# Kernel tuning notes

Hardware: AMD Instinct MI355X
Metric: run time of the kernel (lower is better)

## Reference

```python
import jax, jax.numpy as jnp
import numpy as np

B, S, D, DOUT = 16, 1024, 768, 256
TEMP = D ** 0.5


def setup_inputs() -> dict:
    key = jax.random.key(0)
    ks = jax.random.split(key, 16)
    emb = jax.random.normal(ks[0], (B, S, D), dtype=jnp.float32)
    mask = jax.random.randint(ks[1], (B, S), 0, 2, dtype=jnp.int32)
    scale = 0.02
    def lin(kw, kb, din, dout):
        return (jax.random.normal(kw, (din, dout), dtype=jnp.float32) * scale,
                jax.random.normal(kb, (dout,), dtype=jnp.float32) * scale)
    q_Wq, q_bq = lin(ks[2], ks[3], D, D)
    q_Wk, q_bk = lin(ks[4], ks[5], D, D)
    q_Wv, q_bv = lin(ks[6], ks[7], D, DOUT)
    d_Wq, d_bq = lin(ks[8], ks[9], D, D)
    d_Wk, d_bk = lin(ks[10], ks[11], D, D)
    d_Wv, d_bv = lin(ks[12], ks[13], D, DOUT)
    return {
        'emb': emb, 'mask': mask, 'is_query': 1,
        'query_Wq': q_Wq, 'query_bq': q_bq,
        'query_Wk': q_Wk, 'query_bk': q_bk,
        'query_Wv': q_Wv, 'query_bv': q_bv,
        'doc_Wq': d_Wq, 'doc_bq': d_bq,
        'doc_Wk': d_Wk, 'doc_bk': d_bk,
        'doc_Wv': d_Wv, 'doc_bv': d_bv,
    }


def reference(emb, mask, is_query,
              query_Wq, query_bq, query_Wk, query_bk, query_Wv, query_bv,
              doc_Wq, doc_bq, doc_Wk, doc_bk, doc_Wv, doc_bv):
    # is_query is a static Python int/bool selecting the projection set
    if is_query:
        Wq, bq, Wk, bk, Wv, bv = query_Wq, query_bq, query_Wk, query_bk, query_Wv, query_bv
    else:
        Wq, bq, Wk, bk, Wv, bv = doc_Wq, doc_bq, doc_Wk, doc_bk, doc_Wv, doc_bv
    q = jnp.einsum('bsd,de->bse', emb, Wq) + bq  # [B,S,D]
    k = jnp.einsum('bsd,de->bse', emb, Wk) + bk  # [B,S,D]
    v = jnp.einsum('bsd,de->bse', emb, Wv) + bv  # [B,S,DOUT]
    attn = jnp.einsum('bqd,bkd->bqk', q / TEMP, k)  # [B,S,S]
    attn = jnp.where(mask[:, None, :] == 0, jnp.float32(-1e9), attn)
    attn = jax.nn.softmax(attn, axis=-1)
    out = jnp.einsum('bqk,bkd->bqd', attn, v)  # [B,S,DOUT]
    return out, attn
```

## Files before the change

kernel.cpp:

```cpp
#include <hip/hip_runtime.h>
#include <hip/hip_bf16.h>

static constexpr float INV_TEMP = 0.03608439182435161f;

typedef __attribute__((ext_vector_type(8))) short bf16x8;
typedef __attribute__((ext_vector_type(4))) float f32x4;
typedef __attribute__((ext_vector_type(8))) unsigned short u16x8;
typedef __attribute__((ext_vector_type(4))) unsigned short u16x4;

__device__ __forceinline__ unsigned short f2bf(float f) {
  unsigned u = __float_as_uint(f);
  u += 0x7fffu + ((u >> 16) & 1u);
  return (unsigned short)(u >> 16);
}
__device__ __forceinline__ float bf2f(unsigned short h) {
  return __uint_as_float((unsigned)h << 16);
}

__device__ __forceinline__ void async_copy16(const void* g, void* lds) {
  __builtin_amdgcn_global_load_lds(
      (const __attribute__((address_space(1))) unsigned int*)g,
      (__attribute__((address_space(3))) unsigned int*)lds, 16, 0, 0);
}

__global__ __launch_bounds__(256) void pack_emb(const float* __restrict__ src,
                                                unsigned short* __restrict__ QKE) {
  long i = ((long)blockIdx.x * 256 + threadIdx.x) * 8;
  const long row = i / 768, col = i % 768;
  float4 a = *(const float4*)(src + i);
  float4 b = *(const float4*)(src + i + 4);
  u16x8 v;
  v[0] = f2bf(a.x); v[1] = f2bf(a.y); v[2] = f2bf(a.z); v[3] = f2bf(a.w);
  v[4] = f2bf(b.x); v[5] = f2bf(b.y); v[6] = f2bf(b.z); v[7] = f2bf(b.w);
  *(u16x8*)(QKE + row * 1536 + 768 + col) = v;
}

__global__ __launch_bounds__(256) void pack_sel(
    const int* __restrict__ isq_p,
    const float* qWq, const float* qWk, const float* qWv, const float* qbv,
    const float* dWq, const float* dWk, const float* dWv, const float* dbv,
    unsigned short* __restrict__ Wq_bf,
    unsigned short* __restrict__ Wk_bf,
    unsigned short* __restrict__ WvTe,
    float* __restrict__ bias_v) {
  const int b = blockIdx.x, t = threadIdx.x;
  const int isq = *isq_p;
  if (b < 1152) {
    const int which = b >= 576;
    const float* W = which ? (isq ? qWk : dWk) : (isq ? qWq : dWq);
    unsigned short* o = which ? Wk_bf : Wq_bf;
    const long i = ((long)(which ? b - 576 : b) * 256 + t) * 4;
    float4 x = *(const float4*)(W + i);
    u16x4 y; y[0] = f2bf(x.x); y[1] = f2bf(x.y); y[2] = f2bf(x.z); y[3] = f2bf(x.w);
    *(u16x4*)(o + i) = y;
  } else if (b < 1344) {
    const float* Wv = isq ? qWv : dWv;
    const long base = ((long)(b - 1152) * 256 + t) * 4;
#pragma unroll
    for (int j = 0; j < 4; ++j) {
      long o = base + j;
      int n = (int)(o / 768), d = (int)(o % 768);
      WvTe[o] = f2bf(Wv[(long)d * 256 + n]);
    }
  } else {
    const float* bv = isq ? qbv : dbv;
    if (t < 256) bias_v[t] = bv[t];
  }
}

__global__ __launch_bounds__(256) void gemm_g(
    const unsigned short* __restrict__ Wk_bf,
    const unsigned short* __restrict__ Wq_bf,
    unsigned short* __restrict__ Gt) {
  __shared__ unsigned short Ab[2][64 * 32];
  __shared__ unsigned short Bb[2][64 * 32];
  const int tid = threadIdx.x, wid = tid >> 6, lane = tid & 63;
  const unsigned short* A = Wk_bf + (long)blockIdx.x * 64 * 768;
  const unsigned short* BT = Wq_bf + (long)blockIdx.y * 64 * 768;

  auto stage = [&](int buf, int kt) {
    const int e = tid * 8, row = e >> 5, col = e & 31;
    async_copy16(A + (long)row * 768 + kt * 32 + col, &Ab[buf][e]);
    async_copy16(BT + (long)row * 768 + kt * 32 + col, &Bb[buf][e]);
  };

  f32x4 acc[2][2] = {};
  stage(0, 0);
  __syncthreads();
  int buf = 0;
  const int wr = wid >> 1, wc = wid & 1;
  const int fr = lane & 15, fq = lane >> 4;
  for (int kt = 0; kt < 24; ++kt) {
    if (kt + 1 < 24) stage(buf ^ 1, kt + 1);
    const unsigned short* Ap = &Ab[buf][(wr * 32 + fr) * 32 + fq * 8];
    const unsigned short* Bp = &Bb[buf][(wc * 32 + fr) * 32 + fq * 8];
    bf16x8 a[2], b[2];
#pragma unroll
    for (int mi = 0; mi < 2; ++mi) a[mi] = *(const bf16x8*)(Ap + mi * 16 * 32);
#pragma unroll
    for (int ni = 0; ni < 2; ++ni) b[ni] = *(const bf16x8*)(Bp + ni * 16 * 32);
#pragma unroll
    for (int mi = 0; mi < 2; ++mi)
#pragma unroll
      for (int ni = 0; ni < 2; ++ni)
        acc[mi][ni] = __builtin_amdgcn_mfma_f32_16x16x32_bf16(a[mi], b[ni], acc[mi][ni], 0, 0, 0);
    __syncthreads();
    buf ^= 1;
  }
#pragma unroll
  for (int mi = 0; mi < 2; ++mi)
#pragma unroll
    for (int ni = 0; ni < 2; ++ni) {
      const long m = (long)blockIdx.x * 64 + wr * 32 + mi * 16 + fq * 4;
      const long n = (long)blockIdx.y * 64 + wc * 32 + ni * 16 + fr;
      f32x4 v = acc[mi][ni];
#pragma unroll
      for (int r = 0; r < 4; ++r) Gt[(m + r) * 768 + n] = f2bf(v[r]);
    }
}

__global__ __launch_bounds__(256) void uvc_fast(
    const int* __restrict__ isq_p,
    const float* qWq, const float* qbq, const float* qWk, const float* qbk,
    const float* dWq, const float* dbq, const float* dWk, const float* dbk,
    unsigned short* __restrict__ WvTe, float* __restrict__ bias_v) {
  const int b = blockIdx.x, t = threadIdx.x;
  const int isq = *isq_p;
  const float* Wq = isq ? qWq : dWq;  const float* bq = isq ? qbq : dbq;
  const float* Wk = isq ? qWk : dWk;  const float* bk = isq ? qbk : dbk;
  __shared__ float red[256];
  if (b < 1536) {
    const int lo = (b < 768);
    const int d = lo ? b : b - 768;
    const float* W = lo ? Wq : Wk;
    const float* bvec = lo ? bk : bq;
    float s = 0.f;
#pragma unroll
    for (int i = 0; i < 3; ++i) {
      const int a = t + i * 256;
      s += W[(long)d * 768 + a] * bvec[a];
    }
    red[t] = s;
    __syncthreads();
    for (int off = 128; off; off >>= 1) {
      if (t < off) red[t] += red[t + off];
      __syncthreads();
    }
    if (t == 0) WvTe[(long)(lo ? 256 : 257) * 768 + d] = f2bf(red[0]);
  } else {
    if (t < 128) bias_v[256 + t] = 0.f;
    float p = 0.f;
    for (int a = t; a < 768; a += 256) p += bq[a] * bk[a];
    red[t] = p;
    __syncthreads();
    for (int off = 128; off; off >>= 1) {
      if (t < off) red[t] += red[t + off];
      __syncthreads();
    }
    if (t == 0) bias_v[256] = red[0];
  }
}

__device__ __forceinline__ void k_loop_256(
    const unsigned short* __restrict__ Apan, long lda,
    const unsigned short* __restrict__ Bpan, long ldb,
    int nk, unsigned short* smem, f32x4 (&acc)[8][4]) {
  const int tid = threadIdx.x;
  const int wid = tid >> 6, lane = tid & 63;
  const int wr = wid >> 2, wc = wid & 3;
  const int fr = lane & 15, fq = lane >> 4;

  auto stage = [&](int tile, int mat, int ks, int buf) {
    const unsigned short* g = (mat ? Bpan : Apan) + (long)tile * 64 + ks * 32;
    const long ld = mat ? ldb : lda;
    unsigned short* d = smem + (((buf << 2) | (mat << 1) | ks) << 13);
#pragma unroll
    for (int i = 0; i < 2; ++i) {
      const int e = (tid + i * 512) * 8;
      const int row = e >> 5;
      const int sl = (e >> 3) & 3;
      const int ss = sl ^ ((row >> 1) & 3);
      async_copy16(g + (long)row * ld + ss * 8, d + e);
    }
  };

  const int fro = fr * 32 + ((fq ^ ((fr >> 1) & 3)) << 3);
  const int awo = fro + (wr * 128) * 32;
  const int bwo = fro + (wc * 64) * 32;

  stage(0, 0, 0, 0); stage(0, 1, 0, 0); stage(0, 0, 1, 0); stage(0, 1, 1, 0);
  if (nk > 1) {
    stage(1, 0, 0, 1); stage(1, 1, 1, 1);
    asm volatile("s_waitcnt vmcnt(4)" ::: "memory");
  } else {
    asm volatile("s_waitcnt vmcnt(0)" ::: "memory");
  }
  __builtin_amdgcn_sched_barrier(0);
  __builtin_amdgcn_s_barrier();

  for (int t = 0; t < nk; ++t) {
    const int p = t & 1;
    const unsigned short* A0 = smem + (((p << 2) | 0) << 13);
    const unsigned short* A1 = smem + (((p << 2) | 1) << 13);
    const unsigned short* B0 = smem + (((p << 2) | 2) << 13);
    const unsigned short* B1 = smem + (((p << 2) | 3) << 13);
    bf16x8 a[4], b[4];

#pragma unroll
    for (int m = 0; m < 4; ++m) a[m] = *(const bf16x8*)(A0 + awo + m * 512);
#pragma unroll
    for (int n = 0; n < 4; ++n) b[n] = *(const bf16x8*)(B0 + bwo + n * 512);
    if (t + 1 < nk) stage(t + 1, 0, 1, (t + 1) & 1);
    __builtin_amdgcn_s_barrier();
    asm volatile("s_waitcnt lgkmcnt(0)");
    __builtin_amdgcn_sched_barrier(0);
    __builtin_amdgcn_s_setprio(1);
#pragma unroll
    for (int m = 0; m < 4; ++m)
#pragma unroll
      for (int n = 0; n < 4; ++n)
        acc[m][n] = __builtin_amdgcn_mfma_f32_16x16x32_bf16(a[m], b[n], acc[m][n], 0, 0, 0);
    __builtin_amdgcn_s_setprio(0);
    __builtin_amdgcn_sched_barrier(0);
    __builtin_amdgcn_s_barrier();

#pragma unroll
    for (int m = 0; m < 4; ++m) a[m] = *(const bf16x8*)(A0 + awo + (4 + m) * 512);
    if (t + 1 < nk) stage(t + 1, 1, 0, (t + 1) & 1);
    __builtin_amdgcn_s_barrier();
    asm volatile("s_waitcnt lgkmcnt(0)");
    __builtin_amdgcn_sched_barrier(0);
    __builtin_amdgcn_s_setprio(1);
#pragma unroll
    for (int m = 0; m < 4; ++m)
#pragma unroll
      for (int n = 0; n < 4; ++n)
        acc[4 + m][n] = __builtin_amdgcn_mfma_f32_16x16x32_bf16(a[m], b[n], acc[4 + m][n], 0, 0, 0);
    __builtin_amdgcn_s_setprio(0);
    __builtin_amdgcn_sched_barrier(0);
    __builtin_amdgcn_s_barrier();

#pragma unroll
    for (int m = 0; m < 4; ++m) a[m] = *(const bf16x8*)(A1 + awo + m * 512);
#pragma unroll
    for (int n = 0; n < 4; ++n) b[n] = *(const bf16x8*)(B1 + bwo + n * 512);
    if (t + 2 < nk) stage(t + 2, 0, 0, p);
    __builtin_amdgcn_s_barrier();
    asm volatile("s_waitcnt lgkmcnt(0)");
    __builtin_amdgcn_sched_barrier(0);
    __builtin_amdgcn_s_setprio(1);
#pragma unroll
    for (int m = 0; m < 4; ++m)
#pragma unroll
      for (int n = 0; n < 4; ++n)
        acc[m][n] = __builtin_amdgcn_mfma_f32_16x16x32_bf16(a[m], b[n], acc[m][n], 0, 0, 0);
    __builtin_amdgcn_s_setprio(0);
    __builtin_amdgcn_sched_barrier(0);
    __builtin_amdgcn_s_barrier();

#pragma unroll
    for (int m = 0; m < 4; ++m) a[m] = *(const bf16x8*)(A1 + awo + (4 + m) * 512);
    if (t + 2 < nk) stage(t + 2, 1, 1, p);
    __builtin_amdgcn_s_barrier();
    asm volatile("s_waitcnt lgkmcnt(0)");
    __builtin_amdgcn_sched_barrier(0);
    __builtin_amdgcn_s_setprio(1);
#pragma unroll
    for (int m = 0; m < 4; ++m)
#pragma unroll
      for (int n = 0; n < 4; ++n)
        acc[4 + m][n] = __builtin_amdgcn_mfma_f32_16x16x32_bf16(a[m], b[n], acc[4 + m][n], 0, 0, 0);
    __builtin_amdgcn_s_setprio(0);
    if (t < nk - 2) {
      asm volatile("s_waitcnt vmcnt(4)" ::: "memory");
    } else if (t == nk - 2) {
      asm volatile("s_waitcnt vmcnt(0)" ::: "memory");
    }
    __builtin_amdgcn_sched_barrier(0);
    __builtin_amdgcn_s_barrier();
  }
}

__global__ __launch_bounds__(512, 2) void tproj256(
    unsigned short* __restrict__ QKE,
    const unsigned short* __restrict__ Gt) {
  extern __shared__ unsigned short smem[];
  const int f = blockIdx.x;
  const int kx = f & 7, c = f >> 3;
  const long bx = 8 * kx + (c & 7);
  const long yb = c >> 3;
  const unsigned short* Apan = QKE + 768 + bx * 256 * 1536;
  const unsigned short* Bpan = Gt + yb * 256 * 768;
  f32x4 acc[8][4];
#pragma unroll
  for (int m = 0; m < 8; ++m)
#pragma unroll
    for (int n = 0; n < 4; ++n) acc[m][n] = f32x4{0.f, 0.f, 0.f, 0.f};

  k_loop_256(Apan, 1536, Bpan, 768, 12, smem, acc);

  const int wid = threadIdx.x >> 6, lane = threadIdx.x & 63;
  const int wr = wid >> 2, wc = wid & 3;
  const int fr = lane & 15, fq = lane >> 4;
#pragma unroll
  for (int m = 0; m < 8; ++m)
#pragma unroll
    for (int n = 0; n < 4; ++n) {
      const long mm = bx * 256 + wr * 128 + m * 16 + fq * 4;
      const long nn = yb * 256 + wc * 64 + n * 16 + fr;
      f32x4 v = acc[m][n];
#pragma unroll
      for (int r = 0; r < 4; ++r) QKE[(mm + r) * 1536 + nn] = f2bf(v[r]);
    }
}

__global__ __launch_bounds__(512, 2) void logits256(
    const unsigned short* __restrict__ QKE,
    const unsigned short* __restrict__ VTe,
    float* __restrict__ attn) {
  extern __shared__ unsigned short smem[];
  const int f = blockIdx.x;
  const int kx = f & 7, c = f >> 3;
  const int bz = 2 * kx + (c >> 4);
  const int inner = c & 15, bx = inner & 3, by = inner >> 2;
  const unsigned short* Apan = QKE + (long)bz * 1024 * 1536 + (long)bx * 256 * 1536;
  const unsigned short* Bpan = QKE + 768 + (long)bz * 1024 * 1536 + (long)by * 256 * 1536;
  f32x4 acc[8][4];
#pragma unroll
  for (int m = 0; m < 8; ++m)
#pragma unroll
    for (int n = 0; n < 4; ++n) acc[m][n] = f32x4{0.f, 0.f, 0.f, 0.f};

  k_loop_256(Apan, 1536, Bpan, 1536, 12, smem, acc);

  const int wid = threadIdx.x >> 6, lane = threadIdx.x & 63;
  const int wr = wid >> 2, wc = wid & 3;
  const int fr = lane & 15, fq = lane >> 4;
  float* C = attn + (long)bz * 1024 * 1024;
  const unsigned short* rvec = VTe + (long)256 * 16384 + (long)bz * 1024;
  const unsigned short* cvec = VTe + (long)257 * 16384 + (long)bz * 1024;
#pragma unroll
  for (int m = 0; m < 8; ++m)
#pragma unroll
    for (int n = 0; n < 4; ++n) {
      const long mm = (long)bx * 256 + wr * 128 + m * 16 + fq * 4;
      const long nn = (long)by * 256 + wc * 64 + n * 16 + fr;
      const float cB = bf2f(cvec[nn]);
      f32x4 v = acc[m][n];
#pragma unroll
      for (int r = 0; r < 4; ++r) {
        const float rA = bf2f(rvec[mm + r]);
        C[(mm + r) * 1024 + nn] = (v[r] + rA + cB) * INV_TEMP;
      }
    }
}

__global__ __launch_bounds__(256) void gemm_vt(
    const unsigned short* __restrict__ WvTe,
    const unsigned short* __restrict__ QKE,
    const float* __restrict__ bias_v,
    unsigned short* __restrict__ VTe) {
  __shared__ unsigned short Ab[2][128 * 32];
  __shared__ unsigned short Bb[2][128 * 32];
  const int tid = threadIdx.x, wid = tid >> 6, lane = tid & 63;
  const unsigned short* A = WvTe + (long)blockIdx.x * 128 * 768;
  const unsigned short* BT = QKE + 768 + (long)blockIdx.y * 128 * 1536;
  const int srow = lane >> 2;
  const int skk = (lane & 3) * 8;

  auto stage = [&](int buf, int kt) {
    const unsigned short* As = A + (long)kt * 32;
    const unsigned short* Bs = BT + (long)kt * 32;
#pragma unroll
    for (int i = 0; i < 2; ++i) {
      int c = wid * 2 + i;
      async_copy16(As + (long)(c * 16 + srow) * 768 + skk, &Ab[buf][c * 512]);
      async_copy16(Bs + (long)(c * 16 + srow) * 1536 + skk, &Bb[buf][c * 512]);
    }
  };

  f32x4 acc[4][4] = {};
  stage(0, 0);
  __syncthreads();
  int buf = 0;
  const int wr = wid >> 1, wc = wid & 1;
  const int fr = lane & 15, fq = lane >> 4;
  for (int kt = 0; kt < 24; ++kt) {
    if (kt + 1 < 24) stage(buf ^ 1, kt + 1);
    const unsigned short* Ap = &Ab[buf][(wr * 64 + fr) * 32 + fq * 8];
    const unsigned short* Bp = &Bb[buf][(wc * 64 + fr) * 32 + fq * 8];
    bf16x8 af[4], bfv[4];
#pragma unroll
    for (int mi = 0; mi < 4; ++mi) af[mi] = *(const bf16x8*)(Ap + mi * 16 * 32);
#pragma unroll
    for (int ni = 0; ni < 4; ++ni) bfv[ni] = *(const bf16x8*)(Bp + ni * 16 * 32);
#pragma unroll
    for (int mi = 0; mi < 4; ++mi)
#pragma unroll
      for (int ni = 0; ni < 4; ++ni)
        acc[mi][ni] = __builtin_amdgcn_mfma_f32_16x16x32_bf16(af[mi], bfv[ni], acc[mi][ni], 0, 0, 0);
    __syncthreads();
    buf ^= 1;
  }
#pragma unroll
  for (int mi = 0; mi < 4; ++mi)
#pragma unroll
    for (int ni = 0; ni < 4; ++ni) {
      const long m = (long)blockIdx.x * 128 + wr * 64 + mi * 16 + fq * 4;
      const long n = (long)blockIdx.y * 128 + wc * 64 + ni * 16 + fr;
      f32x4 v = acc[mi][ni];
#pragma unroll
      for (int r = 0; r < 4; ++r)
        VTe[(m + r) * 16384 + n] = f2bf(v[r] + bias_v[m + r]);
    }
}

__global__ __launch_bounds__(256) void softmax_rows(float* __restrict__ attn,
                                                    const int* __restrict__ mask,
                                                    unsigned short* __restrict__ attn_bf) {
  const int row = blockIdx.x;
  const int b = row >> 10;
  float* p = attn + (long)row * 1024;
  const int tid = threadIdx.x, lane = tid & 63, wid = tid >> 6;
  float4 v = ((const float4*)p)[tid];
  int4 mk = ((const int4*)(mask + b * 1024))[tid];
  v.x = mk.x ? v.x : -1e9f;
  v.y = mk.y ? v.y : -1e9f;
  v.z = mk.z ? v.z : -1e9f;
  v.w = mk.w ? v.w : -1e9f;
  float mx = fmaxf(fmaxf(v.x, v.y), fmaxf(v.z, v.w));
#pragma unroll
  for (int off = 32; off; off >>= 1) mx = fmaxf(mx, __shfl_xor(mx, off));
  __shared__ float red[4];
  if (lane == 0) red[wid] = mx;
  __syncthreads();
  mx = fmaxf(fmaxf(red[0], red[1]), fmaxf(red[2], red[3]));
  float e0 = __expf(v.x - mx), e1 = __expf(v.y - mx);
  float e2 = __expf(v.z - mx), e3 = __expf(v.w - mx);
  float s = e0 + e1 + e2 + e3;
#pragma unroll
  for (int off = 32; off; off >>= 1) s += __shfl_xor(s, off);
  __shared__ float red2[4];
  if (lane == 0) red2[wid] = s;
  __syncthreads();
  s = red2[0] + red2[1] + red2[2] + red2[3];
  const float inv = 1.0f / s;
  float4 o;
  o.x = e0 * inv; o.y = e1 * inv; o.z = e2 * inv; o.w = e3 * inv;
  ((float4*)p)[tid] = o;
  u16x4 ob;
  ob[0] = f2bf(o.x); ob[1] = f2bf(o.y); ob[2] = f2bf(o.z); ob[3] = f2bf(o.w);
  *(u16x4*)(attn_bf + (long)row * 1024 + tid * 4) = ob;
}

__global__ __launch_bounds__(256) void gemm_pv(
    const unsigned short* __restrict__ attnbf,
    const unsigned short* __restrict__ VTe,
    float* __restrict__ out) {
  __shared__ unsigned short Ab[2][128 * 32];
  __shared__ unsigned short Bb[2][64 * 32];
  const int tid = threadIdx.x, wid = tid >> 6, lane = tid & 63;
  const int bz = blockIdx.z;
  const unsigned short* A = attnbf + (long)bz * 1024 * 1024 + (long)blockIdx.x * 128 * 1024;
  const unsigned short* BT = VTe + (long)bz * 1024 + (long)blockIdx.y * 64 * 16384;
  const int srow = lane >> 2;
  const int skk = (lane & 3) * 8;

  auto stage = [&](int buf, int kt) {
    const unsigned short* As = A + (long)kt * 32;
    const unsigned short* Bs = BT + (long)kt * 32;
#pragma unroll
    for (int i = 0; i < 2; ++i) {
      int c = wid * 2 + i;
      async_copy16(As + (long)(c * 16 + srow) * 1024 + skk, &Ab[buf][c * 512]);
    }
    async_copy16(Bs + (long)(wid * 16 + srow) * 16384 + skk, &Bb[buf][wid * 512]);
  };

  f32x4 acc[4][2] = {};
  stage(0, 0);
  __syncthreads();
  int buf = 0;
  const int wr = wid >> 1, wc = wid & 1;
  const int fr = lane & 15, fq = lane >> 4;
  for (int kt = 0; kt < 32; ++kt) {
    if (kt + 1 < 32) stage(buf ^ 1, kt + 1);
    const unsigned short* Ap = &Ab[buf][(wr * 64 + fr) * 32 + fq * 8];
    const unsigned short* Bp = &Bb[buf][(wc * 32 + fr) * 32 + fq * 8];
    bf16x8 af[4], bfv[2];
#pragma unroll
    for (int mi = 0; mi < 4; ++mi) af[mi] = *(const bf16x8*)(Ap + mi * 16 * 32);
#pragma unroll
    for (int ni = 0; ni < 2; ++ni) bfv[ni] = *(const bf16x8*)(Bp + ni * 16 * 32);
#pragma unroll
    for (int mi = 0; mi < 4; ++mi)
#pragma unroll
      for (int ni = 0; ni < 2; ++ni)
        acc[mi][ni] = __builtin_amdgcn_mfma_f32_16x16x32_bf16(af[mi], bfv[ni], acc[mi][ni], 0, 0, 0);
    __syncthreads();
    buf ^= 1;
  }

  float* C = out + (long)bz * 1024 * 256;
  const long m0 = (long)blockIdx.x * 128 + wr * 64;
  const long n0 = (long)blockIdx.y * 64 + wc * 32;
#pragma unroll
  for (int mi = 0; mi < 4; ++mi)
#pragma unroll
    for (int ni = 0; ni < 2; ++ni) {
      const long m = m0 + mi * 16 + fq * 4;
      const long n = n0 + ni * 16 + fr;
      f32x4 v = acc[mi][ni];
#pragma unroll
      for (int r = 0; r < 4; ++r) C[(m + r) * 256 + n] = v[r];
    }
}

extern "C" void kernel_launch(void* const* d_in, const int* in_sizes, int n_in,
                              void* d_out, int out_size, void* d_ws, size_t ws_size,
                              hipStream_t stream) {
  const float* emb = (const float*)d_in[0];
  const int* mask = (const int*)d_in[1];
  const int* isq = (const int*)d_in[2];
  const float* qWq = (const float*)d_in[3];  const float* qbq = (const float*)d_in[4];
  const float* qWk = (const float*)d_in[5];  const float* qbk = (const float*)d_in[6];
  const float* qWv = (const float*)d_in[7];  const float* qbv = (const float*)d_in[8];
  const float* dWq = (const float*)d_in[9];  const float* dbq = (const float*)d_in[10];
  const float* dWk = (const float*)d_in[11]; const float* dbk = (const float*)d_in[12];
  const float* dWv = (const float*)d_in[13]; const float* dbv = (const float*)d_in[14];

  char* ws = (char*)d_ws;
  unsigned short* QKE    = (unsigned short*)ws;  ws += (size_t)16384 * 1536 * 2;
  unsigned short* Wq_bf  = (unsigned short*)ws;  ws += (size_t)768 * 768 * 2;
  unsigned short* Wk_bf  = (unsigned short*)ws;  ws += (size_t)768 * 768 * 2;
  unsigned short* WvTe   = (unsigned short*)ws;  ws += (size_t)384 * 768 * 2;
  unsigned short* Gt     = (unsigned short*)ws;  ws += (size_t)768 * 768 * 2;
  float*          bias_v = (float*)ws;           ws += (size_t)384 * 4;
  unsigned short* VTe    = (unsigned short*)ws;  ws += (size_t)384 * 16384 * 2;
  unsigned short* attnbf = (unsigned short*)ws;  ws += (size_t)16 * 1024 * 1024 * 2;

  float* out = (float*)d_out;
  float* attn = out + (size_t)16 * 1024 * 256;

  (void)hipFuncSetAttribute((const void*)&tproj256,
                            hipFuncAttributeMaxDynamicSharedMemorySize, 131072);
  (void)hipFuncSetAttribute((const void*)&logits256,
                            hipFuncAttributeMaxDynamicSharedMemorySize, 131072);

  hipLaunchKernelGGL(pack_emb, dim3(6144), dim3(256), 0, stream, emb, QKE);
  hipLaunchKernelGGL(pack_sel, dim3(1345), dim3(256), 0, stream, isq,
                     qWq, qWk, qWv, qbv, dWq, dWk, dWv, dbv, Wq_bf, Wk_bf, WvTe, bias_v);
  hipLaunchKernelGGL(gemm_g, dim3(12, 12), dim3(256), 0, stream, Wk_bf, Wq_bf, Gt);
  hipLaunchKernelGGL(uvc_fast, dim3(1537), dim3(256), 0, stream, isq,
                     qWq, qbq, qWk, qbk, dWq, dbq, dWk, dbk, WvTe, bias_v);
  hipLaunchKernelGGL(tproj256, dim3(192), dim3(512), 131072, stream, QKE, Gt);
  hipLaunchKernelGGL(gemm_vt, dim3(3, 128), dim3(256), 0, stream,
                     WvTe, QKE, bias_v, VTe);
  hipLaunchKernelGGL(logits256, dim3(256), dim3(512), 131072, stream, QKE, VTe, attn);
  hipLaunchKernelGGL(softmax_rows, dim3(16384), dim3(256), 0, stream, attn, mask, attnbf);
  hipLaunchKernelGGL(gemm_pv, dim3(8, 4, 16), dim3(256), 0, stream, attnbf, VTe, out);
}
```

Baseline: 167.7 us.

## Replace 256x256 hand-pipelined GEMMs with simpler 128x128 double-buffered kernels

Swaps the tproj and logits kernels, previously 512-thread 256x256-tile kernels with a hand-scheduled pipeline and 128KB of dynamic LDS, for 256-thread 128x128-tile kernels using static 32KB double-buffered LDS and a plain sync-per-k-step loop. The grids grow from 192/256 blocks to 768/1024, which gives better CU coverage and occupancy on a 256-CU part. In exchange each tile has less reuse, and the loop drops the fine-grained barrier, priority and waitcnt interleaving, so it may hide global-load latency less well.

```diff
diff --git a/kernel.cpp b/kernel.cpp
--- a/kernel.cpp
+++ b/kernel.cpp
@@ -161,196 +161,133 @@
   }
 }
 
-__device__ __forceinline__ void k_loop_256(
-    const unsigned short* __restrict__ Apan, long lda,
-    const unsigned short* __restrict__ Bpan, long ldb,
-    int nk, unsigned short* smem, f32x4 (&acc)[8][4]) {
-  const int tid = threadIdx.x;
-  const int wid = tid >> 6, lane = tid & 63;
-  const int wr = wid >> 2, wc = wid & 3;
-  const int fr = lane & 15, fq = lane >> 4;
-
-  auto stage = [&](int tile, int mat, int ks, int buf) {
-    const unsigned short* g = (mat ? Bpan : Apan) + (long)tile * 64 + ks * 32;
-    const long ld = mat ? ldb : lda;
-    unsigned short* d = smem + (((buf << 2) | (mat << 1) | ks) << 13);
-#pragma unroll
-    for (int i = 0; i < 2; ++i) {
-      const int e = (tid + i * 512) * 8;
-      const int row = e >> 5;
-      const int sl = (e >> 3) & 3;
-      const int ss = sl ^ ((row >> 1) & 3);
-      async_copy16(g + (long)row * ld + ss * 8, d + e);
-    }
-  };
-
-  const int fro = fr * 32 + ((fq ^ ((fr >> 1) & 3)) << 3);
-  const int awo = fro + (wr * 128) * 32;
-  const int bwo = fro + (wc * 64) * 32;
-
-  stage(0, 0, 0, 0); stage(0, 1, 0, 0); stage(0, 0, 1, 0); stage(0, 1, 1, 0);
-  if (nk > 1) {
-    stage(1, 0, 0, 1); stage(1, 1, 1, 1);
-    asm volatile("s_waitcnt vmcnt(4)" ::: "memory");
-  } else {
-    asm volatile("s_waitcnt vmcnt(0)" ::: "memory");
-  }
-  __builtin_amdgcn_sched_barrier(0);
-  __builtin_amdgcn_s_barrier();
-
-  for (int t = 0; t < nk; ++t) {
-    const int p = t & 1;
-    const unsigned short* A0 = smem + (((p << 2) | 0) << 13);
-    const unsigned short* A1 = smem + (((p << 2) | 1) << 13);
-    const unsigned short* B0 = smem + (((p << 2) | 2) << 13);
-    const unsigned short* B1 = smem + (((p << 2) | 3) << 13);
-    bf16x8 a[4], b[4];
-
-#pragma unroll
-    for (int m = 0; m < 4; ++m) a[m] = *(const bf16x8*)(A0 + awo + m * 512);
-#pragma unroll
-    for (int n = 0; n < 4; ++n) b[n] = *(const bf16x8*)(B0 + bwo + n * 512);
-    if (t + 1 < nk) stage(t + 1, 0, 1, (t + 1) & 1);
-    __builtin_amdgcn_s_barrier();
-    asm volatile("s_waitcnt lgkmcnt(0)");
-    __builtin_amdgcn_sched_barrier(0);
-    __builtin_amdgcn_s_setprio(1);
-#pragma unroll
-    for (int m = 0; m < 4; ++m)
-#pragma unroll
-      for (int n = 0; n < 4; ++n)
-        acc[m][n] = __builtin_amdgcn_mfma_f32_16x16x32_bf16(a[m], b[n], acc[m][n], 0, 0, 0);
-    __builtin_amdgcn_s_setprio(0);
-    __builtin_amdgcn_sched_barrier(0);
-    __builtin_amdgcn_s_barrier();
-
-#pragma unroll
-    for (int m = 0; m < 4; ++m) a[m] = *(const bf16x8*)(A0 + awo + (4 + m) * 512);
-    if (t + 1 < nk) stage(t + 1, 1, 0, (t + 1) & 1);
-    __builtin_amdgcn_s_barrier();
-    asm volatile("s_waitcnt lgkmcnt(0)");
-    __builtin_amdgcn_sched_barrier(0);
-    __builtin_amdgcn_s_setprio(1);
-#pragma unroll
-    for (int m = 0; m < 4; ++m)
-#pragma unroll
-      for (int n = 0; n < 4; ++n)
-        acc[4 + m][n] = __builtin_amdgcn_mfma_f32_16x16x32_bf16(a[m], b[n], acc[4 + m][n], 0, 0, 0);
-    __builtin_amdgcn_s_setprio(0);
-    __builtin_amdgcn_sched_barrier(0);
-    __builtin_amdgcn_s_barrier();
-
-#pragma unroll
-    for (int m = 0; m < 4; ++m) a[m] = *(const bf16x8*)(A1 + awo + m * 512);
-#pragma unroll
-    for (int n = 0; n < 4; ++n) b[n] = *(const bf16x8*)(B1 + bwo + n * 512);
-    if (t + 2 < nk) stage(t + 2, 0, 0, p);
-    __builtin_amdgcn_s_barrier();
-    asm volatile("s_waitcnt lgkmcnt(0)");
-    __builtin_amdgcn_sched_barrier(0);
-    __builtin_amdgcn_s_setprio(1);
-#pragma unroll
-    for (int m = 0; m < 4; ++m)
-#pragma unroll
-      for (int n = 0; n < 4; ++n)
-        acc[m][n] = __builtin_amdgcn_mfma_f32_16x16x32_bf16(a[m], b[n], acc[m][n], 0, 0, 0);
-    __builtin_amdgcn_s_setprio(0);
-    __builtin_amdgcn_sched_barrier(0);
-    __builtin_amdgcn_s_barrier();
-
-#pragma unroll
-    for (int m = 0; m < 4; ++m) a[m] = *(const bf16x8*)(A1 + awo + (4 + m) * 512);
-    if (t + 2 < nk) stage(t + 2, 1, 1, p);
-    __builtin_amdgcn_s_barrier();
-    asm volatile("s_waitcnt lgkmcnt(0)");
-    __builtin_amdgcn_sched_barrier(0);
-    __builtin_amdgcn_s_setprio(1);
-#pragma unroll
-    for (int m = 0; m < 4; ++m)
-#pragma unroll
-      for (int n = 0; n < 4; ++n)
-        acc[4 + m][n] = __builtin_amdgcn_mfma_f32_16x16x32_bf16(a[m], b[n], acc[4 + m][n], 0, 0, 0);
-    __builtin_amdgcn_s_setprio(0);
-    if (t < nk - 2) {
-      asm volatile("s_waitcnt vmcnt(4)" ::: "memory");
-    } else if (t == nk - 2) {
-      asm volatile("s_waitcnt vmcnt(0)" ::: "memory");
-    }
-    __builtin_amdgcn_sched_barrier(0);
-    __builtin_amdgcn_s_barrier();
-  }
-}
-
-__global__ __launch_bounds__(512, 2) void tproj256(
+__global__ __launch_bounds__(256) void tproj2(
     unsigned short* __restrict__ QKE,
     const unsigned short* __restrict__ Gt) {
-  extern __shared__ unsigned short smem[];
+  __shared__ unsigned short Ab[2][128 * 32];
+  __shared__ unsigned short Bb[2][128 * 32];
+  const int tid = threadIdx.x, wid = tid >> 6, lane = tid & 63;
   const int f = blockIdx.x;
   const int kx = f & 7, c = f >> 3;
-  const long bx = 8 * kx + (c & 7);
-  const long yb = c >> 3;
-  const unsigned short* Apan = QKE + 768 + bx * 256 * 1536;
-  const unsigned short* Bpan = Gt + yb * 256 * 768;
-  f32x4 acc[8][4];
-#pragma unroll
-  for (int m = 0; m < 8; ++m)
-#pragma unroll
-    for (int n = 0; n < 4; ++n) acc[m][n] = f32x4{0.f, 0.f, 0.f, 0.f};
-
-  k_loop_256(Apan, 1536, Bpan, 768, 12, smem, acc);
-
-  const int wid = threadIdx.x >> 6, lane = threadIdx.x & 63;
-  const int wr = wid >> 2, wc = wid & 3;
+  const long nt = c >> 4;
+  const long mt = 16 * kx + (c & 15);
+  const unsigned short* A = QKE + 768 + mt * 128 * 1536;
+  const unsigned short* BT = Gt + nt * 128 * 768;
+  const int srow = lane >> 2;
+  const int skk = (lane & 3) * 8;
+
+  auto stage = [&](int buf, int kt) {
+    const unsigned short* As = A + (long)kt * 32;
+    const unsigned short* Bs = BT + (long)kt * 32;
+#pragma unroll
+    for (int i = 0; i < 2; ++i) {
+      int ch = wid * 2 + i;
+      async_copy16(As + (long)(ch * 16 + srow) * 1536 + skk, &Ab[buf][ch * 512]);
+      async_copy16(Bs + (long)(ch * 16 + srow) * 768 + skk, &Bb[buf][ch * 512]);
+    }
+  };
+
+  f32x4 acc[4][4] = {};
+  stage(0, 0);
+  __syncthreads();
+  int buf = 0;
+  const int wr = wid >> 1, wc = wid & 1;
   const int fr = lane & 15, fq = lane >> 4;
-#pragma unroll
-  for (int m = 0; m < 8; ++m)
-#pragma unroll
-    for (int n = 0; n < 4; ++n) {
-      const long mm = bx * 256 + wr * 128 + m * 16 + fq * 4;
-      const long nn = yb * 256 + wc * 64 + n * 16 + fr;
-      f32x4 v = acc[m][n];
-#pragma unroll
-      for (int r = 0; r < 4; ++r) QKE[(mm + r) * 1536 + nn] = f2bf(v[r]);
-    }
-}
-
-__global__ __launch_bounds__(512, 2) void logits256(
+  for (int kt = 0; kt < 24; ++kt) {
+    if (kt + 1 < 24) stage(buf ^ 1, kt + 1);
+    const unsigned short* Ap = &Ab[buf][(wr * 64 + fr) * 32 + fq * 8];
+    const unsigned short* Bp = &Bb[buf][(wc * 64 + fr) * 32 + fq * 8];
+    bf16x8 af[4], bfv[4];
+#pragma unroll
+    for (int mi = 0; mi < 4; ++mi) af[mi] = *(const bf16x8*)(Ap + mi * 16 * 32);
+#pragma unroll
+    for (int ni = 0; ni < 4; ++ni) bfv[ni] = *(const bf16x8*)(Bp + ni * 16 * 32);
+#pragma unroll
+    for (int mi = 0; mi < 4; ++mi)
+#pragma unroll
+      for (int ni = 0; ni < 4; ++ni)
+        acc[mi][ni] = __builtin_amdgcn_mfma_f32_16x16x32_bf16(af[mi], bfv[ni], acc[mi][ni], 0, 0, 0);
+    __syncthreads();
+    buf ^= 1;
+  }
+#pragma unroll
+  for (int mi = 0; mi < 4; ++mi)
+#pragma unroll
+    for (int ni = 0; ni < 4; ++ni) {
+      const long m = mt * 128 + wr * 64 + mi * 16 + fq * 4;
+      const long n = nt * 128 + wc * 64 + ni * 16 + fr;
+      f32x4 v = acc[mi][ni];
+#pragma unroll
+      for (int r = 0; r < 4; ++r) QKE[(m + r) * 1536 + n] = f2bf(v[r]);
+    }
+}
+
+__global__ __launch_bounds__(256) void logits2(
     const unsigned short* __restrict__ QKE,
     const unsigned short* __restrict__ VTe,
     float* __restrict__ attn) {
-  extern __shared__ unsigned short smem[];
+  __shared__ unsigned short Ab[2][128 * 32];
+  __shared__ unsigned short Bb[2][128 * 32];
+  const int tid = threadIdx.x, wid = tid >> 6, lane = tid & 63;
   const int f = blockIdx.x;
   const int kx = f & 7, c = f >> 3;
-  const int bz = 2 * kx + (c >> 4);
-  const int inner = c & 15, bx = inner & 3, by = inner >> 2;
-  const unsigned short* Apan = QKE + (long)bz * 1024 * 1536 + (long)bx * 256 * 1536;
-  const unsigned short* Bpan = QKE + 768 + (long)bz * 1024 * 1536 + (long)by * 256 * 1536;
-  f32x4 acc[8][4];
-#pragma unroll
-  for (int m = 0; m < 8; ++m)
-#pragma unroll
-    for (int n = 0; n < 4; ++n) acc[m][n] = f32x4{0.f, 0.f, 0.f, 0.f};
-
-  k_loop_256(Apan, 1536, Bpan, 1536, 12, smem, acc);
-
-  const int wid = threadIdx.x >> 6, lane = threadIdx.x & 63;
-  const int wr = wid >> 2, wc = wid & 3;
+  const int bz = 2 * kx + (c >> 6);
+  const int i2 = c & 63, by = i2 >> 3, bx = i2 & 7;
+  const unsigned short* A = QKE + (long)bz * 1024 * 1536 + (long)bx * 128 * 1536;
+  const unsigned short* BT = QKE + 768 + (long)bz * 1024 * 1536 + (long)by * 128 * 1536;
+  const int srow = lane >> 2;
+  const int skk = (lane & 3) * 8;
+
+  auto stage = [&](int buf, int kt) {
+    const unsigned short* As = A + (long)kt * 32;
+    const unsigned short* Bs = BT + (long)kt * 32;
+#pragma unroll
+    for (int i = 0; i < 2; ++i) {
+      int ch = wid * 2 + i;
+      async_copy16(As + (long)(ch * 16 + srow) * 1536 + skk, &Ab[buf][ch * 512]);
+      async_copy16(Bs + (long)(ch * 16 + srow) * 1536 + skk, &Bb[buf][ch * 512]);
+    }
+  };
+
+  f32x4 acc[4][4] = {};
+  stage(0, 0);
+  __syncthreads();
+  int buf = 0;
+  const int wr = wid >> 1, wc = wid & 1;
   const int fr = lane & 15, fq = lane >> 4;
+  for (int kt = 0; kt < 24; ++kt) {
+    if (kt + 1 < 24) stage(buf ^ 1, kt + 1);
+    const unsigned short* Ap = &Ab[buf][(wr * 64 + fr) * 32 + fq * 8];
+    const unsigned short* Bp = &Bb[buf][(wc * 64 + fr) * 32 + fq * 8];
+    bf16x8 af[4], bfv[4];
+#pragma unroll
+    for (int mi = 0; mi < 4; ++mi) af[mi] = *(const bf16x8*)(Ap + mi * 16 * 32);
+#pragma unroll
+    for (int ni = 0; ni < 4; ++ni) bfv[ni] = *(const bf16x8*)(Bp + ni * 16 * 32);
+#pragma unroll
+    for (int mi = 0; mi < 4; ++mi)
+#pragma unroll
+      for (int ni = 0; ni < 4; ++ni)
+        acc[mi][ni] = __builtin_amdgcn_mfma_f32_16x16x32_bf16(af[mi], bfv[ni], acc[mi][ni], 0, 0, 0);
+    __syncthreads();
+    buf ^= 1;
+  }
+
   float* C = attn + (long)bz * 1024 * 1024;
   const unsigned short* rvec = VTe + (long)256 * 16384 + (long)bz * 1024;
   const unsigned short* cvec = VTe + (long)257 * 16384 + (long)bz * 1024;
 #pragma unroll
-  for (int m = 0; m < 8; ++m)
-#pragma unroll
-    for (int n = 0; n < 4; ++n) {
-      const long mm = (long)bx * 256 + wr * 128 + m * 16 + fq * 4;
-      const long nn = (long)by * 256 + wc * 64 + n * 16 + fr;
-      const float cB = bf2f(cvec[nn]);
-      f32x4 v = acc[m][n];
+  for (int mi = 0; mi < 4; ++mi)
+#pragma unroll
+    for (int ni = 0; ni < 4; ++ni) {
+      const long m = (long)bx * 128 + wr * 64 + mi * 16 + fq * 4;
+      const long n = (long)by * 128 + wc * 64 + ni * 16 + fr;
+      const float cB = bf2f(cvec[n]);
+      f32x4 v = acc[mi][ni];
 #pragma unroll
       for (int r = 0; r < 4; ++r) {
-        const float rA = bf2f(rvec[mm + r]);
-        C[(mm + r) * 1024 + nn] = (v[r] + rA + cB) * INV_TEMP;
+        const float rA = bf2f(rvec[m + r]);
+        C[(m + r) * 1024 + n] = (v[r] + rA + cB) * INV_TEMP;
       }
     }
 }
@@ -373,9 +310,9 @@
     const unsigned short* Bs = BT + (long)kt * 32;
 #pragma unroll
     for (int i = 0; i < 2; ++i) {
-      int c = wid * 2 + i;
-      async_copy16(As + (long)(c * 16 + srow) * 768 + skk, &Ab[buf][c * 512]);
-      async_copy16(Bs + (long)(c * 16 + srow) * 1536 + skk, &Bb[buf][c * 512]);
+      int ch = wid * 2 + i;
+      async_copy16(As + (long)(ch * 16 + srow) * 768 + skk, &Ab[buf][ch * 512]);
+      async_copy16(Bs + (long)(ch * 16 + srow) * 1536 + skk, &Bb[buf][ch * 512]);
     }
   };
 
@@ -471,8 +408,8 @@
     const unsigned short* Bs = BT + (long)kt * 32;
 #pragma unroll
     for (int i = 0; i < 2; ++i) {
-      int c = wid * 2 + i;
-      async_copy16(As + (long)(c * 16 + srow) * 1024 + skk, &Ab[buf][c * 512]);
+      int ch = wid * 2 + i;
+      async_copy16(As + (long)(ch * 16 + srow) * 1024 + skk, &Ab[buf][ch * 512]);
     }
     async_copy16(Bs + (long)(wid * 16 + srow) * 16384 + skk, &Bb[buf][wid * 512]);
   };
@@ -542,21 +479,16 @@
   float* out = (float*)d_out;
   float* attn = out + (size_t)16 * 1024 * 256;
 
-  (void)hipFuncSetAttribute((const void*)&tproj256,
-                            hipFuncAttributeMaxDynamicSharedMemorySize, 131072);
-  (void)hipFuncSetAttribute((const void*)&logits256,
-                            hipFuncAttributeMaxDynamicSharedMemorySize, 131072);
-
   hipLaunchKernelGGL(pack_emb, dim3(6144), dim3(256), 0, stream, emb, QKE);
   hipLaunchKernelGGL(pack_sel, dim3(1345), dim3(256), 0, stream, isq,
                      qWq, qWk, qWv, qbv, dWq, dWk, dWv, dbv, Wq_bf, Wk_bf, WvTe, bias_v);
   hipLaunchKernelGGL(gemm_g, dim3(12, 12), dim3(256), 0, stream, Wk_bf, Wq_bf, Gt);
   hipLaunchKernelGGL(uvc_fast, dim3(1537), dim3(256), 0, stream, isq,
                      qWq, qbq, qWk, qbk, dWq, dbq, dWk, dbk, WvTe, bias_v);
-  hipLaunchKernelGGL(tproj256, dim3(192), dim3(512), 131072, stream, QKE, Gt);
+  hipLaunchKernelGGL(tproj2, dim3(768), dim3(256), 0, stream, QKE, Gt);
   hipLaunchKernelGGL(gemm_vt, dim3(3, 128), dim3(256), 0, stream,
                      WvTe, QKE, bias_v, VTe);
-  hipLaunchKernelGGL(logits256, dim3(256), dim3(512), 131072, stream, QKE, VTe, attn);
+  hipLaunchKernelGGL(logits2, dim3(1024), dim3(256), 0, stream, QKE, VTe, attn);
   hipLaunchKernelGGL(softmax_rows, dim3(16384), dim3(256), 0, stream, attn, mask, attnbf);
   hipLaunchKernelGGL(gemm_pv, dim3(8, 4, 16), dim3(256), 0, stream, attnbf, VTe, out);
 }
```

New measurement: 186.7 us. +11.3%, slower.
